# Optimization experiments

Hardware: AMD Instinct MI355X
Metric: run time of the kernel (lower is better)

## Reference

```python
import jax, jax.numpy as jnp
import numpy as np

L, B, S, E, H, V = 4, 2, 1024, 1024, 16, 32000
HD = E // H          # head_size = 64
FF = 6 * E           # FeedForward expansion = 6
EPS = 1e-5


def setup_inputs() -> dict:
    key = jax.random.key(0)
    ks = jax.random.split(key, 12)
    std = jnp.float32(0.02)

    def nrm(k, shape):
        return jax.random.normal(k, shape, jnp.float32) * std

    return {
        "x":   jax.random.randint(ks[0], (B, S), 0, V),
        "emb": nrm(ks[1], (V, E)),            # token embedding table
        "pos": nrm(ks[2], (S, E)),            # position embedding table (context = S)
        "Wq":  nrm(ks[3], (L, H, E, HD)),     # per-layer, per-head q Linear (no bias)
        "Wk":  nrm(ks[4], (L, H, E, HD)),
        "Wv":  nrm(ks[5], (L, H, E, HD)),
        "Wo":  nrm(ks[6], (L, E, E)),         # MHA output projection
        "g1":  jnp.ones((L, E), jnp.float32), "b1": jnp.zeros((L, E), jnp.float32),
        "g2":  jnp.ones((L, E), jnp.float32), "b2": jnp.zeros((L, E), jnp.float32),
        "W1":  nrm(ks[7], (L, E, FF)),        # FFN up
        "W2":  nrm(ks[8], (L, FF, E)),        # FFN down
        "gf":  jnp.ones((E,), jnp.float32), "bf": jnp.zeros((E,), jnp.float32),
        "Wf":  nrm(ks[9], (E, V)),            # final LM head (no bias)
    }


def _ln(x, g, b):
    mu = jnp.mean(x, -1, keepdims=True)
    var = jnp.mean((x - mu) ** 2, -1, keepdims=True)
    return (x - mu) * jax.lax.rsqrt(var + EPS) * g + b


def _gpt(x, emb, pos, Wq, Wk, Wv, Wo, g1, b1, g2, b2, W1, W2, gf, bf, Wf):
    Bsz, Sl = x.shape
    h = emb[x] + pos[:Sl]                         # [B,S,E]
    mask = jnp.tril(jnp.ones((Sl, Sl), bool))     # causal 'trill' buffer

    def block(h, p):
        wq, wk, wv, wo, ga, ba, gb, bb, w1, w2 = p
        z = _ln(h, ga, ba)
        q = jnp.einsum('bse,hed->bhsd', z, wq)
        k = jnp.einsum('bse,hed->bhsd', z, wk)
        v = jnp.einsum('bse,hed->bhsd', z, wv)
        att = jnp.einsum('bhsd,bhtd->bhst', q, k) * (HD ** -0.5)
        att = jnp.where(mask, att, -jnp.inf)
        att = jax.nn.softmax(att, axis=-1)
        o = jnp.einsum('bhst,bhtd->bhsd', att, v)
        o = o.transpose(0, 2, 1, 3).reshape(h.shape[0], h.shape[1], E)  # concat heads
        h = h + o @ wo                                                   # residual 1
        z = _ln(h, gb, bb)
        h = h + jax.nn.gelu(z @ w1, approximate=False) @ w2              # residual 2
        return h, None

    h, _ = jax.lax.scan(block, h, (Wq, Wk, Wv, Wo, g1, b1, g2, b2, W1, W2))
    return _ln(h, gf, bf) @ Wf                    # logits [B,S,V]


def reference(x, emb, pos, Wq, Wk, Wv, Wo, g1, b1, g2, b2, W1, W2, gf, bf, Wf):
    return _gpt(x, emb, pos, Wq, Wk, Wv, Wo, g1, b1, g2, b2, W1, W2, gf, bf, Wf)
```

## Files before the change

kernel.cpp:

```cpp
#include <hip/hip_runtime.h>
#include <hip/hip_bf16.h>
#include <math.h>


typedef unsigned short ushort_t;
typedef unsigned short us8 __attribute__((ext_vector_type(8)));
typedef unsigned short us4 __attribute__((ext_vector_type(4)));
typedef __bf16 bf16x8 __attribute__((ext_vector_type(8)));
typedef float f32x4 __attribute__((ext_vector_type(4)));

#define LN_EPS 1e-5f

__device__ inline ushort_t f2bf(float f) {
    union { float f; unsigned u; } v; v.f = f;
    unsigned r = v.u + 0x7FFFu + ((v.u >> 16) & 1u);
    return (ushort_t)(r >> 16);
}

#define GLD_LDS16(gp, lp)                                                  \
    __builtin_amdgcn_global_load_lds(                                      \
        (const __attribute__((address_space(1))) unsigned int*)(gp),       \
        (__attribute__((address_space(3))) unsigned int*)(lp), 16, 0, 0)

enum { EPI_F32 = 0, EPI_BF16 = 1, EPI_ADDF32 = 2, EPI_GELU = 3, EPI_TBF16 = 4,
       EPI_ATOM = 5, EPI_QKV = 6 };

template<int EPI>
__global__ __launch_bounds__(512)
void gemm8p(const ushort_t* __restrict__ A, const ushort_t* __restrict__ B,
            void* __restrict__ Cv, int mt, int K, int lda, int ldb, int ldc,
            long bsA, long bsB, long bsC)
{
    extern __shared__ ushort_t smem[];

    const int nwg  = gridDim.x;
    const int orig = blockIdx.x;
    int wgid = orig;
    if (nwg >= 8) {
        const int q = nwg >> 3, r = nwg & 7;
        const int xcd = orig & 7, i = orig >> 3;
        wgid = (xcd < r ? xcd * (q + 1) : r * (q + 1) + (xcd - r) * q) + i;
    }
    const int m0 = (wgid % mt) * 128;
    const int n0 = (wgid / mt) * 256;

    A += (long)blockIdx.z * bsA;
    B += (long)blockIdx.z * bsB;

    const int tid  = threadIdx.x;
    const int lane = tid & 63;
    const int wid  = tid >> 6;
    const int wm   = wid >> 2, wn = wid & 3;
    const int cg   = lane >> 4, cl = lane & 15;
    const int lr   = lane >> 3;
    const int lcc  = (lane & 7) * 8;

    const int nt = K >> 6;

    auto stage = [&](int kt, int buf, int part) {
        ushort_t* base = smem + buf * 24576;
        const int k0 = kt * 64;
        if (part < 2) {
            const int rbase = part * 64 + wid * 8;
            const int row   = rbase + lr;
            const int col   = lcc ^ ((row & 7) << 3);
            GLD_LDS16(&A[(long)(m0 + row) * lda + k0 + col], base + rbase * 64);
        } else {
            const int rbase = (part - 2) * 64 + wid * 8;
            const int row   = rbase + lr;
            const int col   = lcc ^ ((row & 7) << 3);
            GLD_LDS16(&B[(long)(n0 + row) * ldb + k0 + col],
                      base + 8192 + rbase * 64);
        }
    };

    #pragma unroll
    for (int p = 0; p < 6; ++p) stage(0, 0, p);
    #pragma unroll
    for (int p = 0; p < 6; ++p) stage(1, 1, p);
    asm volatile("s_waitcnt vmcnt(6)" ::: "memory");
    __builtin_amdgcn_s_barrier();

    f32x4 acc[4][4] = {};

    for (int t = 0; t < nt; ++t) {
        const ushort_t* Aq = smem + (t % 3) * 24576;
        const ushort_t* Bq = Aq + 8192;
        const int sbuf = (t + 2) % 3;
        const bool do_stage = (t + 2 < nt);

        bf16x8 breg[4][2];
        #pragma unroll
        for (int p = 0; p < 4; ++p) {
            const int rowA = wm * 64 + p * 16 + cl;
            bf16x8 aA[2];
            #pragma unroll
            for (int kk = 0; kk < 2; ++kk)
                aA[kk] = __builtin_bit_cast(bf16x8, *(const us8*)&Aq[
                    rowA * 64 + ((kk * 32 + cg * 8) ^ ((rowA & 7) << 3))]);
            if (p == 0) {
                #pragma unroll
                for (int nj = 0; nj < 4; ++nj) {
                    const int rowB = wn * 64 + nj * 16 + cl;
                    #pragma unroll
                    for (int kk = 0; kk < 2; ++kk)
                        breg[nj][kk] = __builtin_bit_cast(bf16x8, *(const us8*)&Bq[
                            rowB * 64 + ((kk * 32 + cg * 8) ^ ((rowB & 7) << 3))]);
                }
            }
            if (do_stage) {
                if (p == 0)      { stage(t + 2, sbuf, 0); stage(t + 2, sbuf, 1); }
                else if (p == 1) { stage(t + 2, sbuf, 2); stage(t + 2, sbuf, 3); }
                else if (p == 2) { stage(t + 2, sbuf, 4); }
                else             { stage(t + 2, sbuf, 5); }
            }
            __builtin_amdgcn_s_setprio(1);
            #pragma unroll
            for (int nj = 0; nj < 4; ++nj)
                #pragma unroll
                for (int kk = 0; kk < 2; ++kk)
                    acc[p][nj] = __builtin_amdgcn_mfma_f32_16x16x32_bf16(
                        aA[kk], breg[nj][kk], acc[p][nj], 0, 0, 0);
            __builtin_amdgcn_s_setprio(0);
            __builtin_amdgcn_s_barrier();
        }
        if (do_stage) asm volatile("s_waitcnt vmcnt(6)" ::: "memory");
        else          asm volatile("s_waitcnt vmcnt(0)" ::: "memory");
        __builtin_amdgcn_s_barrier();
    }

    const int rb = m0 + wm * 64 + cg * 4;
    const int cb = n0 + wn * 64 + cl;

    #pragma unroll
    for (int mi = 0; mi < 4; ++mi) {
        #pragma unroll
        for (int nj = 0; nj < 4; ++nj) {
            const int colg = cb + nj * 16;
            if (EPI == EPI_QKV) {
                ushort_t* Q = (ushort_t*)Cv;
                if (n0 < 1024) {
                    #pragma unroll
                    for (int r = 0; r < 4; ++r)
                        Q[(long)(rb + mi * 16 + r) * 1024 + colg] = f2bf(acc[mi][nj][r]);
                } else if (n0 < 2048) {
                    #pragma unroll
                    for (int r = 0; r < 4; ++r)
                        Q[2097152 + (long)(rb + mi * 16 + r) * 1024 + (colg - 1024)] =
                            f2bf(acc[mi][nj][r]);
                } else {
                    ushort_t* Vt = Q + 4194304;
                    const int rowg = rb + mi * 16;
                    const long boff = (long)(rowg >> 10) * 1048576;
                    us4 o4;
                    #pragma unroll
                    for (int r = 0; r < 4; ++r) o4[r] = f2bf(acc[mi][nj][r]);
                    *(us4*)&Vt[boff + (long)(colg - 2048) * 1024 + (rowg & 1023)] = o4;
                }
            } else {
                #pragma unroll
                for (int r = 0; r < 4; ++r) {
                    const int  rowg = rb + mi * 16 + r;
                    const long off  = (long)rowg * ldc + colg;
                    const float val = acc[mi][nj][r];
                    if (EPI == EPI_F32) {
                        ((float*)Cv)[off] = val;
                    } else if (EPI == EPI_GELU) {
                        float g = 0.5f * val * (1.0f + erff(val * 0.70710678118654752f));
                        ((ushort_t*)Cv)[off] = f2bf(g);
                    } else if (EPI == EPI_ATOM) {
                        atomicAdd(&((float*)Cv)[off], val);
                    } else {
                        ((ushort_t*)Cv)[off] = f2bf(val);
                    }
                }
            }
        }
    }
}

template<int EPI, int MT>
__global__ __launch_bounds__(256)
void gemm128(const ushort_t* __restrict__ A, const ushort_t* __restrict__ B,
             void* __restrict__ Cv, int K, int lda, int ldb, int ldc,
             long bsA, long bsB, long bsC)
{
    const int m0 = blockIdx.x * (MT * 32);
    const int n0 = blockIdx.y * 128;
    A += (long)blockIdx.z * bsA;
    B += (long)blockIdx.z * bsB;

    __shared__ __align__(16) ushort_t As[MT * 32][64];
    __shared__ __align__(16) ushort_t Bs[128][64];

    const int tid  = threadIdx.x;
    const int lane = tid & 63;
    const int wid  = tid >> 6;
    const int wr   = wid >> 1, wc = wid & 1;
    const int lr   = lane >> 3;
    const int lc   = (lane & 7) * 8;
    const int cg   = lane >> 4;
    const int cl   = lane & 15;

    f32x4 acc[MT][4] = {};

    for (int k0 = 0; k0 < K; k0 += 64) {
        #pragma unroll
        for (int j = 0; j < MT; ++j) {
            const int r = wid * (8 * MT) + j * 8;
            GLD_LDS16(&A[(long)(m0 + r + lr) * lda + k0 + lc], &As[r][0]);
        }
        #pragma unroll
        for (int j = 0; j < 4; ++j) {
            const int r = wid * 32 + j * 8;
            GLD_LDS16(&B[(long)(n0 + r + lr) * ldb + k0 + lc], &Bs[r][0]);
        }
        __syncthreads();
        #pragma unroll
        for (int kk = 0; kk < 2; ++kk) {
            const int krd = kk * 32 + cg * 8;
            bf16x8 af[MT], bfr[4];
            #pragma unroll
            for (int mi = 0; mi < MT; ++mi)
                af[mi] = __builtin_bit_cast(bf16x8,
                    *(const us8*)&As[wr * (MT * 16) + mi * 16 + cl][krd]);
            #pragma unroll
            for (int nj = 0; nj < 4; ++nj)
                bfr[nj] = __builtin_bit_cast(bf16x8,
                    *(const us8*)&Bs[wc * 64 + nj * 16 + cl][krd]);
            #pragma unroll
            for (int mi = 0; mi < MT; ++mi)
                #pragma unroll
                for (int nj = 0; nj < 4; ++nj)
                    acc[mi][nj] = __builtin_amdgcn_mfma_f32_16x16x32_bf16(
                        af[mi], bfr[nj], acc[mi][nj], 0, 0, 0);
        }
        __syncthreads();
    }

    const int rb = m0 + wr * (MT * 16) + cg * 4;
    const int cb = n0 + wc * 64 + cl;

    #pragma unroll
    for (int mi = 0; mi < MT; ++mi)
        #pragma unroll
        for (int nj = 0; nj < 4; ++nj)
            #pragma unroll
            for (int r = 0; r < 4; ++r) {
                const long off = (long)(rb + mi * 16 + r) * ldc + cb + nj * 16;
                const float val = acc[mi][nj][r];
                if (EPI == EPI_ADDF32)      ((float*)Cv)[off] += val;
                else if (EPI == EPI_F32)    ((float*)Cv)[off] = val;
                else                        ((ushort_t*)Cv)[off] = f2bf(val);
            }
}

__global__ __launch_bounds__(256)
void flash_attn(const ushort_t* __restrict__ qb, const ushort_t* __restrict__ kb,
                const ushort_t* __restrict__ vT, ushort_t* __restrict__ ob)
{
    const int qt = gridDim.x - 1 - blockIdx.x;
    const int hh = blockIdx.y;
    const int bb = blockIdx.z;
    const int lane = threadIdx.x & 63;
    const int w    = threadIdx.x >> 6;
    const int cg   = lane >> 4;
    const int cl   = lane & 15;

    __shared__ __align__(16) ushort_t P_lds[4][16][72];

    const int q0 = qt * 64;
    const long tokQ = (long)bb * 1024 + q0 + w * 16 + cl;

    bf16x8 qf[2];
    #pragma unroll
    for (int kk = 0; kk < 2; ++kk)
        qf[kk] = __builtin_bit_cast(bf16x8,
            *(const us8*)&qb[tokQ * 1024 + hh * 64 + kk * 32 + cg * 8]);

    const ushort_t* kbase = kb + (long)bb * 1048576 + hh * 64;
    const ushort_t* vbase = vT + (long)bb * 1048576 + (long)hh * 65536;

    f32x4 o[4] = {};
    float m4[4], l4[4];
    #pragma unroll
    for (int r = 0; r < 4; ++r) { m4[r] = -1e30f; l4[r] = 0.0f; }

    for (int tt = 0; tt <= qt; ++tt) {
        const int t0 = tt * 64;
        f32x4 s[4] = {};
        __builtin_amdgcn_s_setprio(1);
        #pragma unroll
        for (int nj = 0; nj < 4; ++nj) {
            const ushort_t* kp = kbase + (long)(t0 + nj * 16 + cl) * 1024 + cg * 8;
            bf16x8 kf0 = __builtin_bit_cast(bf16x8, *(const us8*)kp);
            bf16x8 kf1 = __builtin_bit_cast(bf16x8, *(const us8*)(kp + 32));
            s[nj] = __builtin_amdgcn_mfma_f32_16x16x32_bf16(qf[0], kf0, s[nj], 0, 0, 0);
            s[nj] = __builtin_amdgcn_mfma_f32_16x16x32_bf16(qf[1], kf1, s[nj], 0, 0, 0);
        }
        __builtin_amdgcn_s_setprio(0);
        const bool diag = (tt == qt);
        float pm[4] = {-3e30f, -3e30f, -3e30f, -3e30f};
        #pragma unroll
        for (int nj = 0; nj < 4; ++nj)
            #pragma unroll
            for (int r = 0; r < 4; ++r) {
                float v = s[nj][r] * 0.125f;
                if (diag && (t0 + nj * 16 + cl) > (q0 + w * 16 + cg * 4 + r))
                    v = -1e30f;
                s[nj][r] = v;
                pm[r] = fmaxf(pm[r], v);
            }
        #pragma unroll
        for (int r = 0; r < 4; ++r)
            #pragma unroll
            for (int msk = 1; msk < 16; msk <<= 1)
                pm[r] = fmaxf(pm[r], __shfl_xor(pm[r], msk));
        float al[4], ps[4];
        #pragma unroll
        for (int r = 0; r < 4; ++r) {
            const float mn = fmaxf(m4[r], pm[r]);
            al[r] = __expf(m4[r] - mn);
            m4[r] = mn;
            ps[r] = 0.0f;
        }
        #pragma unroll
        for (int nj = 0; nj < 4; ++nj)
            #pragma unroll
            for (int r = 0; r < 4; ++r) {
                const float p = __expf(s[nj][r] - m4[r]);
                s[nj][r] = p;
                ps[r] += p;
            }
        #pragma unroll
        for (int r = 0; r < 4; ++r) {
            #pragma unroll
            for (int msk = 1; msk < 16; msk <<= 1)
                ps[r] += __shfl_xor(ps[r], msk);
            l4[r] = l4[r] * al[r] + ps[r];
        }
        #pragma unroll
        for (int nj = 0; nj < 4; ++nj)
            #pragma unroll
            for (int r = 0; r < 4; ++r) o[nj][r] *= al[r];
        #pragma unroll
        for (int nj = 0; nj < 4; ++nj)
            #pragma unroll
            for (int r = 0; r < 4; ++r)
                P_lds[w][cg * 4 + r][nj * 16 + cl] = f2bf(s[nj][r]);
        asm volatile("s_waitcnt lgkmcnt(0)" ::: "memory");
        __builtin_amdgcn_sched_barrier(0);
        bf16x8 pa[2];
        #pragma unroll
        for (int kk = 0; kk < 2; ++kk)
            pa[kk] = __builtin_bit_cast(bf16x8,
                *(const us8*)&P_lds[w][cl][kk * 32 + cg * 8]);
        __builtin_amdgcn_s_setprio(1);
        #pragma unroll
        for (int nj = 0; nj < 4; ++nj) {
            const ushort_t* vp = vbase + (long)(nj * 16 + cl) * 1024 + t0 + cg * 8;
            bf16x8 vf0 = __builtin_bit_cast(bf16x8, *(const us8*)vp);
            bf16x8 vf1 = __builtin_bit_cast(bf16x8, *(const us8*)(vp + 32));
            o[nj] = __builtin_amdgcn_mfma_f32_16x16x32_bf16(pa[0], vf0, o[nj], 0, 0, 0);
            o[nj] = __builtin_amdgcn_mfma_f32_16x16x32_bf16(pa[1], vf1, o[nj], 0, 0, 0);
        }
        __builtin_amdgcn_s_setprio(0);
    }

    #pragma unroll
    for (int r = 0; r < 4; ++r) {
        const float inv = 1.0f / l4[r];
        const long tok = (long)bb * 1024 + q0 + w * 16 + cg * 4 + r;
        #pragma unroll
        for (int nj = 0; nj < 4; ++nj)
            ob[tok * 1024 + hh * 64 + nj * 16 + cl] = f2bf(o[nj][r] * inv);
    }
}

__global__ __launch_bounds__(256)
void transpose_conv(const float* __restrict__ in, ushort_t* __restrict__ out,
                    long ldin, long ldout, long bsin, long bsout,
                    long bsout_hi, int zmod)
{
    __shared__ float tile[32][33];
    const int tx = threadIdx.x, ty = threadIdx.y;
    const long bin  = (long)blockIdx.z * bsin;
    const long bout = (long)(blockIdx.z % zmod) * bsout
                    + (long)(blockIdx.z / zmod) * bsout_hi;
    const int n0 = blockIdx.x * 32, k0 = blockIdx.y * 32;
    #pragma unroll
    for (int i = 0; i < 4; ++i)
        tile[ty + i * 8][tx] = in[bin + (long)(k0 + ty + i * 8) * ldin + n0 + tx];
    __syncthreads();
    #pragma unroll
    for (int i = 0; i < 4; ++i) {
        const int n = ty + i * 8;
        out[bout + (long)(n0 + n) * ldout + k0 + tx] = f2bf(tile[tx][n]);
    }
}

__global__ __launch_bounds__(256)
void embed_kernel(const int* __restrict__ x, const float* __restrict__ emb,
                  const float* __restrict__ pos, float* __restrict__ h)
{
    const int row = blockIdx.x, tid = threadIdx.x;
    const int s = row & 1023;
    const int idx = x[row];
    const float4 e = ((const float4*)(emb + (long)idx * 1024))[tid];
    const float4 p = ((const float4*)(pos + (long)s * 1024))[tid];
    float4 o; o.x = e.x + p.x; o.y = e.y + p.y; o.z = e.z + p.z; o.w = e.w + p.w;
    ((float4*)(h + (long)row * 1024))[tid] = o;
}

__global__ __launch_bounds__(256)
void ln_kernel(const float* __restrict__ x, const float* __restrict__ g,
               const float* __restrict__ b, ushort_t* __restrict__ z)
{
    const int row = blockIdx.x, tid = threadIdx.x;
    const float4 v = ((const float4*)(x + (long)row * 1024))[tid];
    float s  = v.x + v.y + v.z + v.w;
    float sq = v.x * v.x + v.y * v.y + v.z * v.z + v.w * v.w;
    #pragma unroll
    for (int o = 32; o > 0; o >>= 1) { s += __shfl_down(s, o); sq += __shfl_down(sq, o); }
    __shared__ float ls[4], lq[4];
    if ((tid & 63) == 0) { ls[tid >> 6] = s; lq[tid >> 6] = sq; }
    __syncthreads();
    s  = ls[0] + ls[1] + ls[2] + ls[3];
    sq = lq[0] + lq[1] + lq[2] + lq[3];
    const float mu   = s * (1.0f / 1024.0f);
    const float var  = sq * (1.0f / 1024.0f) - mu * mu;
    const float rstd = rsqrtf(var + LN_EPS);
    const float4 gg = ((const float4*)g)[tid];
    const float4 bb = ((const float4*)b)[tid];
    us4 o4;
    o4[0] = f2bf((v.x - mu) * rstd * gg.x + bb.x);
    o4[1] = f2bf((v.y - mu) * rstd * gg.y + bb.y);
    o4[2] = f2bf((v.z - mu) * rstd * gg.z + bb.z);
    o4[3] = f2bf((v.w - mu) * rstd * gg.w + bb.w);
    *(us4*)(z + (long)row * 1024 + tid * 4) = o4;
}

extern "C" void kernel_launch(void* const* d_in, const int* in_sizes, int n_in,
                              void* d_out, int out_size, void* d_ws, size_t ws_size,
                              hipStream_t stream)
{
    const int*   x   = (const int*)  d_in[0];
    const float* emb = (const float*)d_in[1];
    const float* pos = (const float*)d_in[2];
    const float* Wq  = (const float*)d_in[3];
    const float* Wk  = (const float*)d_in[4];
    const float* Wv  = (const float*)d_in[5];
    const float* Wo  = (const float*)d_in[6];
    const float* g1  = (const float*)d_in[7];
    const float* b1  = (const float*)d_in[8];
    const float* g2  = (const float*)d_in[9];
    const float* b2  = (const float*)d_in[10];
    const float* W1  = (const float*)d_in[11];
    const float* W2  = (const float*)d_in[12];
    const float* gf  = (const float*)d_in[13];
    const float* bfp = (const float*)d_in[14];
    const float* Wf  = (const float*)d_in[15];
    float* out = (float*)d_out;

    char* ws = (char*)d_ws;
    size_t off = 0;
    auto alloc = [&](size_t bytes) {
        char* p = ws + off;
        off = (off + bytes + 255) & ~(size_t)255;
        return p;
    };
    ushort_t* WqkvT = (ushort_t*)alloc(4UL * 3145728 * 2);
    ushort_t* WoT   = (ushort_t*)alloc(4UL * 1048576 * 2);
    ushort_t* W1T   = (ushort_t*)alloc(4UL * 6291456 * 2);
    ushort_t* W2T   = (ushort_t*)alloc(4UL * 6291456 * 2);
    ushort_t* WfT   = (ushort_t*)alloc(32768000UL * 2);
    float*    h     = (float*)   alloc(2048UL * 1024 * 4);
    ushort_t* z     = (ushort_t*)alloc(2048UL * 1024 * 2);
    ushort_t* qb    = (ushort_t*)alloc(3UL * 2048 * 1024 * 2);
    ushort_t* kb    = qb + 2097152;
    ushort_t* vT    = qb + 4194304;
    ushort_t* ob    = (ushort_t*)alloc(2048UL * 1024 * 2);
    ushort_t* ub    = (ushort_t*)alloc(2048UL * 6144 * 2);
    (void)ws_size; (void)in_sizes; (void)n_in; (void)out_size;

    const int LDSB = 3 * 49152;
    hipFuncSetAttribute((const void*)&gemm8p<EPI_F32>,
                        hipFuncAttributeMaxDynamicSharedMemorySize, LDSB);
    hipFuncSetAttribute((const void*)&gemm8p<EPI_GELU>,
                        hipFuncAttributeMaxDynamicSharedMemorySize, LDSB);
    hipFuncSetAttribute((const void*)&gemm8p<EPI_ATOM>,
                        hipFuncAttributeMaxDynamicSharedMemorySize, LDSB);
    hipFuncSetAttribute((const void*)&gemm8p<EPI_QKV>,
                        hipFuncAttributeMaxDynamicSharedMemorySize, LDSB);

    const dim3 tb(32, 8);
    transpose_conv<<<dim3(2,   32, 64), tb, 0, stream>>>(Wq, WqkvT,           64, 1024, 65536, 65536, 3145728, 16);
    transpose_conv<<<dim3(2,   32, 64), tb, 0, stream>>>(Wk, WqkvT + 1048576, 64, 1024, 65536, 65536, 3145728, 16);
    transpose_conv<<<dim3(2,   32, 64), tb, 0, stream>>>(Wv, WqkvT + 2097152, 64, 1024, 65536, 65536, 3145728, 16);
    transpose_conv<<<dim3(32,  32,  4), tb, 0, stream>>>(Wo, WoT, 1024,  1024, 1048576, 1048576, 0, 4);
    transpose_conv<<<dim3(192, 32,  4), tb, 0, stream>>>(W1, W1T, 6144,  1024, 6291456, 6291456, 0, 4);
    transpose_conv<<<dim3(32, 192,  4), tb, 0, stream>>>(W2, W2T, 1024,  6144, 6291456, 6291456, 0, 4);
    transpose_conv<<<dim3(1000,32,  1), tb, 0, stream>>>(Wf, WfT, 32000, 1024, 0,       0,       0, 1);

    embed_kernel<<<2048, 256, 0, stream>>>(x, emb, pos, h);

    for (int l = 0; l < 4; ++l) {
        const size_t wsq = (size_t)l * 1048576;
        const size_t wff = (size_t)l * 6291456;

        ln_kernel<<<2048, 256, 0, stream>>>(h, g1 + l * 1024, b1 + l * 1024, z);

        gemm8p<EPI_QKV><<<dim3(16 * 12, 1, 1), 512, LDSB, stream>>>(
            z, WqkvT + (size_t)l * 3145728, qb, 16, 1024, 1024, 1024, 0, 0, 0, 0);

        flash_attn<<<dim3(16, 16, 2), 256, 0, stream>>>(qb, kb, vT, ob);

        gemm128<EPI_ADDF32, 2><<<dim3(32, 8), 256, 0, stream>>>(
            ob, WoT + wsq, h, 1024, 1024, 1024, 1024, 0, 0, 0);

        ln_kernel<<<2048, 256, 0, stream>>>(h, g2 + l * 1024, b2 + l * 1024, z);

        gemm8p<EPI_GELU><<<dim3(16 * 24, 1, 1), 512, LDSB, stream>>>(
            z, W1T + wff, ub, 16, 1024, 1024, 1024, 6144, 0, 0, 0);
        gemm8p<EPI_ATOM><<<dim3(16 * 4, 1, 4), 512, LDSB, stream>>>(
            ub, W2T + wff, h, 16, 1536, 6144, 6144, 1024, 1536, 1536, 0);
    }

    ln_kernel<<<2048, 256, 0, stream>>>(h, gf, bfp, z);
    gemm8p<EPI_F32><<<dim3(16 * 125, 1, 1), 512, LDSB, stream>>>(
        z, WfT, out, 16, 1024, 1024, 1024, 32000, 0, 0, 0);
}
```

Before: 1.230 ms.

## Replace 128x256 triple-buffered GEMM with templated 256x256 double-buffered tile

The main GEMM is generalized to a templated tile height: 256x256 for FFN-up, FFN-down and the LM head, and 128x256 for QKV. The pipeline drops from three LDS buffers with fine-grained staging interleaved into the MFMA loop to two buffers, with one full-tile prefetch per k-step and a full vmcnt(0) wait plus barrier. FFN-down split-K goes from 4 to 8 slices to keep the grid filled. The larger tiles raise reuse per LDS load, but they add register pressure, halve the number of workgroups, and make the memory wait less overlapped with compute.

```diff
diff --git a/kernel.cpp b/kernel.cpp
--- a/kernel.cpp
+++ b/kernel.cpp
@@ -25,12 +25,14 @@
 enum { EPI_F32 = 0, EPI_BF16 = 1, EPI_ADDF32 = 2, EPI_GELU = 3, EPI_TBF16 = 4,
        EPI_ATOM = 5, EPI_QKV = 6 };
 
-template<int EPI>
+template<int EPI, int MFR>
 __global__ __launch_bounds__(512)
-void gemm8p(const ushort_t* __restrict__ A, const ushort_t* __restrict__ B,
-            void* __restrict__ Cv, int mt, int K, int lda, int ldb, int ldc,
-            long bsA, long bsB, long bsC)
-{
+void gemm256(const ushort_t* __restrict__ A, const ushort_t* __restrict__ B,
+             void* __restrict__ Cv, int mt, int K, int lda, int ldb, int ldc,
+             long bsA, long bsB)
+{
+    constexpr int BM   = MFR * 32;
+    constexpr int BUFE = (BM + 256) * 64;
     extern __shared__ ushort_t smem[];
 
     const int nwg  = gridDim.x;
@@ -41,7 +43,7 @@
         const int xcd = orig & 7, i = orig >> 3;
         wgid = (xcd < r ? xcd * (q + 1) : r * (q + 1) + (xcd - r) * q) + i;
     }
-    const int m0 = (wgid % mt) * 128;
+    const int m0 = (wgid % mt) * BM;
     const int n0 = (wgid / mt) * 256;
 
     A += (long)blockIdx.z * bsA;
@@ -52,117 +54,107 @@
     const int wid  = tid >> 6;
     const int wm   = wid >> 2, wn = wid & 3;
     const int cg   = lane >> 4, cl = lane & 15;
-    const int lr   = lane >> 3;
-    const int lcc  = (lane & 7) * 8;
 
     const int nt = K >> 6;
 
-    auto stage = [&](int kt, int buf, int part) {
-        ushort_t* base = smem + buf * 24576;
+    auto stage = [&](int kt) {
+        ushort_t* base = smem + (kt & 1) * BUFE;
         const int k0 = kt * 64;
-        if (part < 2) {
-            const int rbase = part * 64 + wid * 8;
-            const int row   = rbase + lr;
-            const int col   = lcc ^ ((row & 7) << 3);
-            GLD_LDS16(&A[(long)(m0 + row) * lda + k0 + col], base + rbase * 64);
-        } else {
-            const int rbase = (part - 2) * 64 + wid * 8;
-            const int row   = rbase + lr;
-            const int col   = lcc ^ ((row & 7) << 3);
-            GLD_LDS16(&B[(long)(n0 + row) * ldb + k0 + col],
-                      base + 8192 + rbase * 64);
+        #pragma unroll
+        for (int p = 0; p < MFR / 2; ++p) {
+            const int chunk = p * 512 + tid;
+            const int row = chunk >> 3, ch = chunk & 7;
+            GLD_LDS16(&A[(long)(m0 + row) * lda + k0 + ((ch ^ (row & 7)) * 8)],
+                      base + chunk * 8);
+        }
+        #pragma unroll
+        for (int p = 0; p < 4; ++p) {
+            const int chunk = p * 512 + tid;
+            const int row = chunk >> 3, ch = chunk & 7;
+            GLD_LDS16(&B[(long)(n0 + row) * ldb + k0 + ((ch ^ (row & 7)) * 8)],
+                      base + BM * 64 + chunk * 8);
         }
     };
 
-    #pragma unroll
-    for (int p = 0; p < 6; ++p) stage(0, 0, p);
-    #pragma unroll
-    for (int p = 0; p < 6; ++p) stage(1, 1, p);
-    asm volatile("s_waitcnt vmcnt(6)" ::: "memory");
+    stage(0);
+    stage(1);
+    if constexpr (MFR == 8) asm volatile("s_waitcnt vmcnt(8)" ::: "memory");
+    else                    asm volatile("s_waitcnt vmcnt(6)" ::: "memory");
     __builtin_amdgcn_s_barrier();
 
-    f32x4 acc[4][4] = {};
+    f32x4 acc[MFR][4] = {};
 
     for (int t = 0; t < nt; ++t) {
-        const ushort_t* Aq = smem + (t % 3) * 24576;
-        const ushort_t* Bq = Aq + 8192;
-        const int sbuf = (t + 2) % 3;
-        const bool do_stage = (t + 2 < nt);
+        const ushort_t* Aq = smem + (t & 1) * BUFE;
+        const ushort_t* Bq = Aq + BM * 64;
+        if (t >= 1 && t + 1 < nt) stage(t + 1);
 
         bf16x8 breg[4][2];
         #pragma unroll
-        for (int p = 0; p < 4; ++p) {
-            const int rowA = wm * 64 + p * 16 + cl;
-            bf16x8 aA[2];
+        for (int nf = 0; nf < 4; ++nf) {
+            const int rowB = wn * 64 + nf * 16 + cl;
             #pragma unroll
             for (int kk = 0; kk < 2; ++kk)
-                aA[kk] = __builtin_bit_cast(bf16x8, *(const us8*)&Aq[
-                    rowA * 64 + ((kk * 32 + cg * 8) ^ ((rowA & 7) << 3))]);
-            if (p == 0) {
-                #pragma unroll
-                for (int nj = 0; nj < 4; ++nj) {
-                    const int rowB = wn * 64 + nj * 16 + cl;
-                    #pragma unroll
-                    for (int kk = 0; kk < 2; ++kk)
-                        breg[nj][kk] = __builtin_bit_cast(bf16x8, *(const us8*)&Bq[
-                            rowB * 64 + ((kk * 32 + cg * 8) ^ ((rowB & 7) << 3))]);
-                }
+                breg[nf][kk] = __builtin_bit_cast(bf16x8, *(const us8*)&Bq[
+                    rowB * 64 + (((kk * 4 + cg) ^ (rowB & 7)) * 8)]);
+        }
+        __builtin_amdgcn_s_setprio(1);
+        #pragma unroll
+        for (int mf = 0; mf < MFR; ++mf) {
+            const int rowA = wm * (MFR * 16) + mf * 16 + cl;
+            bf16x8 a0 = __builtin_bit_cast(bf16x8, *(const us8*)&Aq[
+                rowA * 64 + ((cg ^ (rowA & 7)) * 8)]);
+            bf16x8 a1 = __builtin_bit_cast(bf16x8, *(const us8*)&Aq[
+                rowA * 64 + (((4 + cg) ^ (rowA & 7)) * 8)]);
+            #pragma unroll
+            for (int nf = 0; nf < 4; ++nf) {
+                acc[mf][nf] = __builtin_amdgcn_mfma_f32_16x16x32_bf16(
+                    a0, breg[nf][0], acc[mf][nf], 0, 0, 0);
+                acc[mf][nf] = __builtin_amdgcn_mfma_f32_16x16x32_bf16(
+                    a1, breg[nf][1], acc[mf][nf], 0, 0, 0);
             }
-            if (do_stage) {
-                if (p == 0)      { stage(t + 2, sbuf, 0); stage(t + 2, sbuf, 1); }
-                else if (p == 1) { stage(t + 2, sbuf, 2); stage(t + 2, sbuf, 3); }
-                else if (p == 2) { stage(t + 2, sbuf, 4); }
-                else             { stage(t + 2, sbuf, 5); }
-            }
-            __builtin_amdgcn_s_setprio(1);
-            #pragma unroll
-            for (int nj = 0; nj < 4; ++nj)
-                #pragma unroll
-                for (int kk = 0; kk < 2; ++kk)
-                    acc[p][nj] = __builtin_amdgcn_mfma_f32_16x16x32_bf16(
-                        aA[kk], breg[nj][kk], acc[p][nj], 0, 0, 0);
-            __builtin_amdgcn_s_setprio(0);
+        }
+        __builtin_amdgcn_s_setprio(0);
+        if (t + 1 < nt) {
+            asm volatile("s_waitcnt vmcnt(0) lgkmcnt(0)" ::: "memory");
             __builtin_amdgcn_s_barrier();
         }
-        if (do_stage) asm volatile("s_waitcnt vmcnt(6)" ::: "memory");
-        else          asm volatile("s_waitcnt vmcnt(0)" ::: "memory");
-        __builtin_amdgcn_s_barrier();
-    }
-
-    const int rb = m0 + wm * 64 + cg * 4;
+    }
+
+    const int rb = m0 + wm * (MFR * 16) + cg * 4;
     const int cb = n0 + wn * 64 + cl;
 
     #pragma unroll
-    for (int mi = 0; mi < 4; ++mi) {
-        #pragma unroll
-        for (int nj = 0; nj < 4; ++nj) {
-            const int colg = cb + nj * 16;
+    for (int mf = 0; mf < MFR; ++mf) {
+        #pragma unroll
+        for (int nf = 0; nf < 4; ++nf) {
+            const int colg = cb + nf * 16;
             if (EPI == EPI_QKV) {
                 ushort_t* Q = (ushort_t*)Cv;
                 if (n0 < 1024) {
                     #pragma unroll
                     for (int r = 0; r < 4; ++r)
-                        Q[(long)(rb + mi * 16 + r) * 1024 + colg] = f2bf(acc[mi][nj][r]);
+                        Q[(long)(rb + mf * 16 + r) * 1024 + colg] = f2bf(acc[mf][nf][r]);
                 } else if (n0 < 2048) {
                     #pragma unroll
                     for (int r = 0; r < 4; ++r)
-                        Q[2097152 + (long)(rb + mi * 16 + r) * 1024 + (colg - 1024)] =
-                            f2bf(acc[mi][nj][r]);
+                        Q[2097152 + (long)(rb + mf * 16 + r) * 1024 + (colg - 1024)] =
+                            f2bf(acc[mf][nf][r]);
                 } else {
                     ushort_t* Vt = Q + 4194304;
-                    const int rowg = rb + mi * 16;
+                    const int rowg = rb + mf * 16;
                     const long boff = (long)(rowg >> 10) * 1048576;
                     us4 o4;
                     #pragma unroll
-                    for (int r = 0; r < 4; ++r) o4[r] = f2bf(acc[mi][nj][r]);
+                    for (int r = 0; r < 4; ++r) o4[r] = f2bf(acc[mf][nf][r]);
                     *(us4*)&Vt[boff + (long)(colg - 2048) * 1024 + (rowg & 1023)] = o4;
                 }
             } else {
                 #pragma unroll
                 for (int r = 0; r < 4; ++r) {
-                    const int  rowg = rb + mi * 16 + r;
+                    const int  rowg = rb + mf * 16 + r;
                     const long off  = (long)rowg * ldc + colg;
-                    const float val = acc[mi][nj][r];
+                    const float val = acc[mf][nf][r];
                     if (EPI == EPI_F32) {
                         ((float*)Cv)[off] = val;
                     } else if (EPI == EPI_GELU) {
@@ -182,13 +174,10 @@
 template<int EPI, int MT>
 __global__ __launch_bounds__(256)
 void gemm128(const ushort_t* __restrict__ A, const ushort_t* __restrict__ B,
-             void* __restrict__ Cv, int K, int lda, int ldb, int ldc,
-             long bsA, long bsB, long bsC)
+             void* __restrict__ Cv, int K, int lda, int ldb, int ldc)
 {
     const int m0 = blockIdx.x * (MT * 32);
     const int n0 = blockIdx.y * 128;
-    A += (long)blockIdx.z * bsA;
-    B += (long)blockIdx.z * bsB;
 
     __shared__ __align__(16) ushort_t As[MT * 32][64];
     __shared__ __align__(16) ushort_t Bs[128][64];
@@ -483,15 +472,16 @@
     ushort_t* ub    = (ushort_t*)alloc(2048UL * 6144 * 2);
     (void)ws_size; (void)in_sizes; (void)n_in; (void)out_size;
 
-    const int LDSB = 3 * 49152;
-    hipFuncSetAttribute((const void*)&gemm8p<EPI_F32>,
-                        hipFuncAttributeMaxDynamicSharedMemorySize, LDSB);
-    hipFuncSetAttribute((const void*)&gemm8p<EPI_GELU>,
-                        hipFuncAttributeMaxDynamicSharedMemorySize, LDSB);
-    hipFuncSetAttribute((const void*)&gemm8p<EPI_ATOM>,
-                        hipFuncAttributeMaxDynamicSharedMemorySize, LDSB);
-    hipFuncSetAttribute((const void*)&gemm8p<EPI_QKV>,
-                        hipFuncAttributeMaxDynamicSharedMemorySize, LDSB);
+    const int LDS8 = 2 * (256 + 256) * 64 * 2;
+    const int LDS4 = 2 * (128 + 256) * 64 * 2;
+    hipFuncSetAttribute((const void*)&gemm256<EPI_F32, 8>,
+                        hipFuncAttributeMaxDynamicSharedMemorySize, LDS8);
+    hipFuncSetAttribute((const void*)&gemm256<EPI_GELU, 8>,
+                        hipFuncAttributeMaxDynamicSharedMemorySize, LDS8);
+    hipFuncSetAttribute((const void*)&gemm256<EPI_ATOM, 8>,
+                        hipFuncAttributeMaxDynamicSharedMemorySize, LDS8);
+    hipFuncSetAttribute((const void*)&gemm256<EPI_QKV, 4>,
+                        hipFuncAttributeMaxDynamicSharedMemorySize, LDS4);
 
     const dim3 tb(32, 8);
     transpose_conv<<<dim3(2,   32, 64), tb, 0, stream>>>(Wq, WqkvT,           64, 1024, 65536, 65536, 3145728, 16);
@@ -505,28 +495,27 @@
     embed_kernel<<<2048, 256, 0, stream>>>(x, emb, pos, h);
 
     for (int l = 0; l < 4; ++l) {
-        const size_t wsq = (size_t)l * 1048576;
         const size_t wff = (size_t)l * 6291456;
 
         ln_kernel<<<2048, 256, 0, stream>>>(h, g1 + l * 1024, b1 + l * 1024, z);
 
-        gemm8p<EPI_QKV><<<dim3(16 * 12, 1, 1), 512, LDSB, stream>>>(
-            z, WqkvT + (size_t)l * 3145728, qb, 16, 1024, 1024, 1024, 0, 0, 0, 0);
+        gemm256<EPI_QKV, 4><<<dim3(16 * 12), 512, LDS4, stream>>>(
+            z, WqkvT + (size_t)l * 3145728, qb, 16, 1024, 1024, 1024, 0, 0, 0);
 
         flash_attn<<<dim3(16, 16, 2), 256, 0, stream>>>(qb, kb, vT, ob);
 
         gemm128<EPI_ADDF32, 2><<<dim3(32, 8), 256, 0, stream>>>(
-            ob, WoT + wsq, h, 1024, 1024, 1024, 1024, 0, 0, 0);
+            ob, WoT + (size_t)l * 1048576, h, 1024, 1024, 1024, 1024);
 
         ln_kernel<<<2048, 256, 0, stream>>>(h, g2 + l * 1024, b2 + l * 1024, z);
 
-        gemm8p<EPI_GELU><<<dim3(16 * 24, 1, 1), 512, LDSB, stream>>>(
-            z, W1T + wff, ub, 16, 1024, 1024, 1024, 6144, 0, 0, 0);
-        gemm8p<EPI_ATOM><<<dim3(16 * 4, 1, 4), 512, LDSB, stream>>>(
-            ub, W2T + wff, h, 16, 1536, 6144, 6144, 1024, 1536, 1536, 0);
+        gemm256<EPI_GELU, 8><<<dim3(8 * 24), 512, LDS8, stream>>>(
+            z, W1T + wff, ub, 8, 1024, 1024, 1024, 6144, 0, 0);
+        gemm256<EPI_ATOM, 8><<<dim3(8 * 4, 1, 8), 512, LDS8, stream>>>(
+            ub, W2T + wff, h, 8, 768, 6144, 6144, 1024, 768, 768);
     }
 
     ln_kernel<<<2048, 256, 0, stream>>>(h, gf, bfp, z);
-    gemm8p<EPI_F32><<<dim3(16 * 125, 1, 1), 512, LDSB, stream>>>(
-        z, WfT, out, 16, 1024, 1024, 1024, 32000, 0, 0, 0);
-}
+    gemm256<EPI_F32, 8><<<dim3(8 * 125), 512, LDS8, stream>>>(
+        z, WfT, out, 8, 1024, 1024, 1024, 32000, 0, 0);
+}
```

After: 1.267 ms. +3.0%, slower.

## Add 256x256-tile 8-wave GEMM with interleaved double-buffered prefetch for FFN-up and LM head

Applied to the files above, without the earlier changes.

Adds a new GEMM kernel with 256x256 output tiles, 8 waves, a double-buffered XOR-swizzled LDS layout, and global-to-LDS prefetch interleaved with the MFMA phases. It replaces the 128-row gemm8p for the GELU FFN-up projection and the final LM-head GEMM. The larger tiles raise arithmetic intensity and cut redundant operand loads. The cost is far fewer workgroups (192 for FFN-up) and higher register pressure from the 8x4 accumulator tiles. It also trims unused batch-stride arguments from gemm128.

```diff
diff --git a/kernel.cpp b/kernel.cpp
--- a/kernel.cpp
+++ b/kernel.cpp
@@ -24,6 +24,153 @@
 
 enum { EPI_F32 = 0, EPI_BF16 = 1, EPI_ADDF32 = 2, EPI_GELU = 3, EPI_TBF16 = 4,
        EPI_ATOM = 5, EPI_QKV = 6 };
+
+template<int EPI>
+__global__ __launch_bounds__(512)
+void gemm8ph(const ushort_t* __restrict__ A, const ushort_t* __restrict__ B,
+             void* __restrict__ Cv, int mt, int K, int lda, int ldb, int ldc)
+{
+    extern __shared__ ushort_t smem[];
+
+    const int nwg  = gridDim.x;
+    const int orig = blockIdx.x;
+    int wgid = orig;
+    if (nwg >= 8) {
+        const int q = nwg >> 3, r = nwg & 7;
+        const int xcd = orig & 7, i = orig >> 3;
+        wgid = (xcd < r ? xcd * (q + 1) : r * (q + 1) + (xcd - r) * q) + i;
+    }
+    const int m0 = (wgid % mt) * 256;
+    const int n0 = (wgid / mt) * 256;
+
+    const int tid  = threadIdx.x;
+    const int lane = tid & 63;
+    const int wid  = tid >> 6;
+    const int wm   = wid >> 2, wn = wid & 3;
+    const int cg   = lane >> 4, cl = lane & 15;
+
+    const int nt = K >> 6;
+    const int ni = nt >> 1;
+
+    auto stageA = [&](int t, int h) {
+        ushort_t* dst = smem + (t & 1) * 32768 + h * 8192;
+        const int k0 = t * 64;
+        #pragma unroll
+        for (int q = 0; q < 2; ++q) {
+            const int slot = q * 512 + tid;
+            const int r = slot >> 3, pc = slot & 7;
+            const int col = (pc ^ (r & 7)) * 8;
+            GLD_LDS16(&A[(long)(m0 + h * 128 + r) * lda + k0 + col], dst + slot * 8);
+        }
+    };
+    auto stageB = [&](int t, int h) {
+        ushort_t* dst = smem + (t & 1) * 32768 + 16384 + h * 8192;
+        const int k0 = t * 64;
+        #pragma unroll
+        for (int q = 0; q < 2; ++q) {
+            const int slot = q * 512 + tid;
+            const int r = slot >> 3, pc = slot & 7;
+            const int col = (pc ^ (r & 7)) * 8;
+            GLD_LDS16(&B[(long)(n0 + h * 128 + r) * ldb + k0 + col], dst + slot * 8);
+        }
+    };
+
+    stageA(0, 0); stageA(0, 1);
+    stageB(0, 0); stageB(0, 1);
+    stageB(1, 0); stageB(1, 1);
+    asm volatile("s_waitcnt vmcnt(4)" ::: "memory");
+    __builtin_amdgcn_s_barrier();
+
+    f32x4 acc[8][4] = {};
+    bf16x8 breg[4][2];
+
+    for (int i = 0; i < ni; ++i) {
+        const int te = 2 * i, to = te + 1;
+        const bool nl = (i + 1 < ni);
+
+        #pragma unroll
+        for (int p = 0; p < 8; ++p) {
+            const int t = (p < 4) ? te : to;
+            const int q = p & 3;
+            const ushort_t* Ar = smem + (t & 1) * 32768;
+            const ushort_t* Br = Ar + 16384;
+
+            if (q == 0) {
+                #pragma unroll
+                for (int nf = 0; nf < 4; ++nf) {
+                    const int rb = wn * 64 + nf * 16 + cl;
+                    #pragma unroll
+                    for (int kk = 0; kk < 2; ++kk)
+                        breg[nf][kk] = __builtin_bit_cast(bf16x8, *(const us8*)&Br[
+                            rb * 64 + (((kk * 4 + cg) ^ (rb & 7)) * 8)]);
+                }
+            }
+            bf16x8 af[2][2];
+            #pragma unroll
+            for (int mi = 0; mi < 2; ++mi) {
+                const int ra = wm * 128 + q * 32 + mi * 16 + cl;
+                #pragma unroll
+                for (int kk = 0; kk < 2; ++kk)
+                    af[mi][kk] = __builtin_bit_cast(bf16x8, *(const us8*)&Ar[
+                        ra * 64 + (((kk * 4 + cg) ^ (ra & 7)) * 8)]);
+            }
+
+            if (p == 0)      { stageA(to, 0); }
+            else if (p == 1) { stageA(to, 1); if (nl) stageB(te + 2, 0); }
+            else if (p == 2) { if (nl) stageB(te + 2, 1); }
+            else if (p == 4) { if (nl) stageA(te + 2, 0); }
+            else if (p == 5) { if (nl) stageA(te + 2, 1); }
+            else if (p == 6) { if (nl) stageB(to + 2, 0); }
+            else if (p == 7) { if (nl) stageB(to + 2, 1); }
+
+            __builtin_amdgcn_s_barrier();
+            asm volatile("s_waitcnt lgkmcnt(0)" ::: "memory");
+            __builtin_amdgcn_s_setprio(1);
+            #pragma unroll
+            for (int mi = 0; mi < 2; ++mi)
+                #pragma unroll
+                for (int nf = 0; nf < 4; ++nf)
+                    #pragma unroll
+                    for (int kk = 0; kk < 2; ++kk)
+                        acc[q * 2 + mi][nf] = __builtin_amdgcn_mfma_f32_16x16x32_bf16(
+                            af[mi][kk], breg[nf][kk], acc[q * 2 + mi][nf], 0, 0, 0);
+            __builtin_amdgcn_s_setprio(0);
+
+            if (p == 3) {
+                if (nl) asm volatile("s_waitcnt vmcnt(4)" ::: "memory");
+                else    asm volatile("s_waitcnt vmcnt(0)" ::: "memory");
+            } else if (p == 7 && nl) {
+                asm volatile("s_waitcnt vmcnt(4)" ::: "memory");
+            }
+            __builtin_amdgcn_s_barrier();
+        }
+    }
+
+    const int rb = m0 + wm * 128 + cg * 4;
+    const int cb = n0 + wn * 64 + cl;
+
+    #pragma unroll
+    for (int mf = 0; mf < 8; ++mf) {
+        #pragma unroll
+        for (int nf = 0; nf < 4; ++nf) {
+            const int colg = cb + nf * 16;
+            #pragma unroll
+            for (int r = 0; r < 4; ++r) {
+                const int  rowg = rb + mf * 16 + r;
+                const long off  = (long)rowg * ldc + colg;
+                const float val = acc[mf][nf][r];
+                if (EPI == EPI_F32) {
+                    ((float*)Cv)[off] = val;
+                } else if (EPI == EPI_GELU) {
+                    float g = 0.5f * val * (1.0f + erff(val * 0.70710678118654752f));
+                    ((ushort_t*)Cv)[off] = f2bf(g);
+                } else {
+                    ((ushort_t*)Cv)[off] = f2bf(val);
+                }
+            }
+        }
+    }
+}
 
 template<int EPI>
 __global__ __launch_bounds__(512)
@@ -182,13 +329,10 @@
 template<int EPI, int MT>
 __global__ __launch_bounds__(256)
 void gemm128(const ushort_t* __restrict__ A, const ushort_t* __restrict__ B,
-             void* __restrict__ Cv, int K, int lda, int ldb, int ldc,
-             long bsA, long bsB, long bsC)
+             void* __restrict__ Cv, int K, int lda, int ldb, int ldc)
 {
     const int m0 = blockIdx.x * (MT * 32);
     const int n0 = blockIdx.y * 128;
-    A += (long)blockIdx.z * bsA;
-    B += (long)blockIdx.z * bsB;
 
     __shared__ __align__(16) ushort_t As[MT * 32][64];
     __shared__ __align__(16) ushort_t Bs[128][64];
@@ -483,15 +627,16 @@
     ushort_t* ub    = (ushort_t*)alloc(2048UL * 6144 * 2);
     (void)ws_size; (void)in_sizes; (void)n_in; (void)out_size;
 
-    const int LDSB = 3 * 49152;
-    hipFuncSetAttribute((const void*)&gemm8p<EPI_F32>,
-                        hipFuncAttributeMaxDynamicSharedMemorySize, LDSB);
-    hipFuncSetAttribute((const void*)&gemm8p<EPI_GELU>,
-                        hipFuncAttributeMaxDynamicSharedMemorySize, LDSB);
+    const int LDS8P = 2 * 32768 * 2;
+    const int LDS3B = 3 * 49152;
+    hipFuncSetAttribute((const void*)&gemm8ph<EPI_F32>,
+                        hipFuncAttributeMaxDynamicSharedMemorySize, LDS8P);
+    hipFuncSetAttribute((const void*)&gemm8ph<EPI_GELU>,
+                        hipFuncAttributeMaxDynamicSharedMemorySize, LDS8P);
+    hipFuncSetAttribute((const void*)&gemm8p<EPI_QKV>,
+                        hipFuncAttributeMaxDynamicSharedMemorySize, LDS3B);
     hipFuncSetAttribute((const void*)&gemm8p<EPI_ATOM>,
-                        hipFuncAttributeMaxDynamicSharedMemorySize, LDSB);
-    hipFuncSetAttribute((const void*)&gemm8p<EPI_QKV>,
-                        hipFuncAttributeMaxDynamicSharedMemorySize, LDSB);
+                        hipFuncAttributeMaxDynamicSharedMemorySize, LDS3B);
 
     const dim3 tb(32, 8);
     transpose_conv<<<dim3(2,   32, 64), tb, 0, stream>>>(Wq, WqkvT,           64, 1024, 65536, 65536, 3145728, 16);
@@ -505,28 +650,27 @@
     embed_kernel<<<2048, 256, 0, stream>>>(x, emb, pos, h);
 
     for (int l = 0; l < 4; ++l) {
-        const size_t wsq = (size_t)l * 1048576;
         const size_t wff = (size_t)l * 6291456;
 
         ln_kernel<<<2048, 256, 0, stream>>>(h, g1 + l * 1024, b1 + l * 1024, z);
 
-        gemm8p<EPI_QKV><<<dim3(16 * 12, 1, 1), 512, LDSB, stream>>>(
-            z, WqkvT + (size_t)l * 3145728, qb, 16, 1024, 1024, 1024, 0, 0, 0, 0);
+        gemm8p<EPI_QKV><<<dim3(16 * 12), 512, LDS3B, stream>>>(
+            z, WqkvT + (size_t)l * 3145728, qb, 16, 1024, 1024, 1024, 1024, 0, 0, 0);
 
         flash_attn<<<dim3(16, 16, 2), 256, 0, stream>>>(qb, kb, vT, ob);
 
         gemm128<EPI_ADDF32, 2><<<dim3(32, 8), 256, 0, stream>>>(
-            ob, WoT + wsq, h, 1024, 1024, 1024, 1024, 0, 0, 0);
+            ob, WoT + (size_t)l * 1048576, h, 1024, 1024, 1024, 1024);
 
         ln_kernel<<<2048, 256, 0, stream>>>(h, g2 + l * 1024, b2 + l * 1024, z);
 
-        gemm8p<EPI_GELU><<<dim3(16 * 24, 1, 1), 512, LDSB, stream>>>(
-            z, W1T + wff, ub, 16, 1024, 1024, 1024, 6144, 0, 0, 0);
-        gemm8p<EPI_ATOM><<<dim3(16 * 4, 1, 4), 512, LDSB, stream>>>(
+        gemm8ph<EPI_GELU><<<dim3(8 * 24), 512, LDS8P, stream>>>(
+            z, W1T + wff, ub, 8, 1024, 1024, 1024, 6144);
+        gemm8p<EPI_ATOM><<<dim3(16 * 4, 1, 4), 512, LDS3B, stream>>>(
             ub, W2T + wff, h, 16, 1536, 6144, 6144, 1024, 1536, 1536, 0);
     }
 
     ln_kernel<<<2048, 256, 0, stream>>>(h, gf, bfp, z);
-    gemm8p<EPI_F32><<<dim3(16 * 125, 1, 1), 512, LDSB, stream>>>(
-        z, WfT, out, 16, 1024, 1024, 1024, 32000, 0, 0, 0);
-}
+    gemm8ph<EPI_F32><<<dim3(8 * 125), 512, LDS8P, stream>>>(
+        z, WfT, out, 8, 1024, 1024, 1024, 32000);
+}
```

Result: faster. 1.173 ms (-4.6%).
